# Optimization experiments

Hardware: AMD Instinct MI355X
Metric: run time of the kernel (lower is better)

The kernel has to match this reference:

```python
import jax, jax.numpy as jnp
import numpy as np

N, C, H, W = 8, 192, 112, 112
TEMPERATURE = 0.1


def setup_inputs() -> dict:
    key = jax.random.key(0)
    k1, k2 = jax.random.split(key)
    features = jax.random.normal(k1, (N, C, H, W), dtype=jnp.float32)
    # Raw per-pixel directions in {-1, 0, 1}; clip the neighbor coordinate into
    # bounds and recompute the direction so EVERY neighbor is valid. The torch
    # module's broadcasting (labels[:, i, j] vs an (N, M) gather) only works when
    # all N neighbors are valid at each pixel, so this matches its assumptions.
    raw = jax.random.randint(k2, (N, 2, H, W), -1, 2)
    ii = jnp.arange(H)[None, :, None]
    jj = jnp.arange(W)[None, None, :]
    d0 = jnp.clip(ii + raw[:, 0], 0, H - 1) - ii
    d1 = jnp.clip(jj + raw[:, 1], 0, W - 1) - jj
    directions = jnp.stack([d0, d1], axis=1).astype(jnp.int32)
    # Single-class labels: the original loss is -inf whenever any mask entry is 0
    # (log of exactly 0), so a finite, comparable baseline needs matching labels.
    labels = jnp.zeros((N, H, W), dtype=jnp.int32)
    return {"features": features, "labels": labels, "directions": directions}


def reference(features, labels, directions):
    # F.normalize(features, dim=1): x / max(||x||_2, eps)
    norm = jnp.linalg.norm(features, axis=1, keepdims=True)
    fn = features / jnp.maximum(norm, 1e-12)

    ii = jnp.arange(H)[None, :, None]
    jj = jnp.arange(W)[None, None, :]
    ni = ii + directions[:, 0]  # (N, H, W), in-bounds by construction
    nj = jj + directions[:, 1]  # (N, H, W)

    # Torch: features[:, :, neighbor_i, neighbor_j] gathers the M(==N) neighbor
    # coordinates across ALL batch elements -> (N, C, N, H, W) = [n, c, m, i, j]
    gathered = fn[:, :, ni, nj]
    # logits[n, m, i, j] = <fn[n, :, i, j], fn[n, :, ni[m,i,j], nj[m,i,j]]> / T
    logits = jnp.einsum('ncij,ncmij->nmij', fn, gathered) / TEMPERATURE

    # mask[n, m, i, j] = (labels[m, i, j] == labels[n, ni[m,i,j], nj[m,i,j]])
    # (torch broadcasts labels[:, i, j] along the first axis of the (N, M) gather)
    labels_g = labels[:, ni, nj]  # (N, N, H, W) = [n, m, i, j]
    mask = (labels[None, :, :, :] == labels_g).astype(fn.dtype)

    exp_l = jnp.exp(logits) * mask
    denom = jnp.sum(exp_l, axis=1, keepdims=True)  # sum over m
    # sum_{i,j} mean_{n,m}(.) / (H*W) == global mean over (n, m, i, j)
    loss = (-jnp.log(exp_l / (denom + 1e-6))).mean()
    return loss
```

## Files before the change

### kernel.cpp

```cpp
#include <hip/hip_runtime.h>
#include <math.h>


namespace {
constexpr int N_ = 8, C_ = 192, H_ = 112, W_ = 112;
constexpr int HW = H_ * W_;
constexpr int TH = 2;
constexpr int WSX = 56;
constexpr int TROWS = TH + 2;
constexpr int RS = WSX + 2;
constexpr int TILE_E = TROWS * RS;
constexpr int NT = 64;
constexpr int NS4 = TILE_E - 3 * NT;
constexpr int NPAIR = TH * (WSX / 2);
constexpr int KCH = 8;
constexpr int GRP = KCH / 2;
constexpr int NCHUNK = C_ / KCH;
constexpr int GX = W_ / WSX, GY = H_ / TH;
constexpr int NBLK = GX * GY * N_;
constexpr float INV_T = 10.0f;
constexpr double TOTAL = (double)N_ * N_ * H_ * W_;
}

__device__ __forceinline__ float sel3(int d, float a, float b, float c) {
    float r = (d < 0) ? a : b;
    return (d > 0) ? c : r;
}

__device__ __forceinline__ float px_loss(
    const float l[3][3], int gi, int gj, int n,
    const int* __restrict__ labels, const int* __restrict__ dirs)
{
    const int pix = gi * W_ + gj;
    float denom = 0.f, sumlog = 0.f;
#pragma unroll
    for (int m = 0; m < N_; ++m) {
        int d0 = dirs[((m * 2 + 0) * H_ + gi) * W_ + gj];
        int d1 = dirs[((m * 2 + 1) * H_ + gi) * W_ + gj];
        float r0 = sel3(d1, l[0][0], l[0][1], l[0][2]);
        float r1 = sel3(d1, l[1][0], l[1][1], l[1][2]);
        float r2 = sel3(d1, l[2][0], l[2][1], l[2][2]);
        float lm = sel3(d0, r0, r1, r2);
        int labm = labels[m * HW + pix];
        int labn = labels[n * HW + (gi + d0) * W_ + (gj + d1)];
        bool msk = (labm == labn);
        float e = msk ? __expf(lm) : 0.f;
        denom += e;
        sumlog += msk ? lm : -INFINITY;
    }
    return 8.0f * __logf(denom + 1e-6f) - sumlog;
}

extern "C" __global__ void __launch_bounds__(NT, 4)
dcl_main(const float* __restrict__ feat,
         const int* __restrict__ labels,
         const int* __restrict__ dirs,
         double* __restrict__ partial, int use_partial)
{
    alignas(16) __shared__ float2 tl[2 * GRP * TILE_E];
    __shared__ float ssb[TILE_E];

    const int lane = threadIdx.x;
    const int gx0 = blockIdx.x * WSX;
    const int gy0 = blockIdx.y * TH;
    const int n   = blockIdx.z;

    const bool has4 = (lane < NS4);
    int gofs[4];
    #pragma unroll
    for (int sI = 0; sI < 4; ++sI) {
        int s = lane + sI * NT;
        if (s >= TILE_E) s = TILE_E - 1;
        int r = s / RS, c = s - r * RS;
        gofs[sI] = min(max(gy0 + r - 1, 0), H_ - 1) * W_
                 + min(max(gx0 + c - 1, 0), W_ - 1);
    }

    const bool is_px = (lane < NPAIR);
    const int py  = lane / (WSX / 2);
    const int pxp = lane - py * (WSX / 2);
    const int wb  = py * RS + 2 * pxp;

    const float* __restrict__ plane = feat + (size_t)n * C_ * HW;

#define TLP(buf, g) (tl + ((buf) * GRP + (g)) * TILE_E)

    float sA[9], sB[9];
    #pragma unroll
    for (int k = 0; k < 9; ++k) { sA[k] = 0.f; sB[k] = 0.f; }
    float ss[4] = {0.f, 0.f, 0.f, 0.f};

    {
        float v[4][KCH];
        #pragma unroll
        for (int k = 0; k < KCH; ++k) {
            v[0][k] = plane[(size_t)k * HW + gofs[0]];
            v[1][k] = plane[(size_t)k * HW + gofs[1]];
            v[2][k] = plane[(size_t)k * HW + gofs[2]];
        }
        if (has4)
            #pragma unroll
            for (int k = 0; k < KCH; ++k) v[3][k] = plane[(size_t)k * HW + gofs[3]];
        #pragma unroll
        for (int g = 0; g < GRP; ++g) {
            TLP(0, g)[lane]            = make_float2(v[0][2*g], v[0][2*g+1]);
            TLP(0, g)[lane + NT]       = make_float2(v[1][2*g], v[1][2*g+1]);
            TLP(0, g)[lane + 2 * NT]   = make_float2(v[2][2*g], v[2][2*g+1]);
        }
        if (has4)
            #pragma unroll
            for (int g = 0; g < GRP; ++g)
                TLP(0, g)[lane + 3 * NT] = make_float2(v[3][2*g], v[3][2*g+1]);
        #pragma unroll
        for (int k = 0; k < KCH; ++k) {
            ss[0] = fmaf(v[0][k], v[0][k], ss[0]);
            ss[1] = fmaf(v[1][k], v[1][k], ss[1]);
            ss[2] = fmaf(v[2][k], v[2][k], ss[2]);
            if (has4) ss[3] = fmaf(v[3][k], v[3][k], ss[3]);
        }
    }
    __syncthreads();

    for (int t = 0; t < NCHUNK; ++t) {
        float v[4][KCH];
        const bool more = (t + 1 < NCHUNK);
        if (more) {
            const float* p = plane + (size_t)(t + 1) * KCH * HW;
            #pragma unroll
            for (int k = 0; k < KCH; ++k) {
                v[0][k] = p[(size_t)k * HW + gofs[0]];
                v[1][k] = p[(size_t)k * HW + gofs[1]];
                v[2][k] = p[(size_t)k * HW + gofs[2]];
            }
            if (has4)
                #pragma unroll
                for (int k = 0; k < KCH; ++k) v[3][k] = p[(size_t)k * HW + gofs[3]];
        }

        const int buf = t & 1;
        if (is_px) {
            #pragma unroll
            for (int g = 0; g < GRP; ++g) {
                const float2* __restrict__ cp = TLP(buf, g);
                float4 L0 = *reinterpret_cast<const float4*>(cp + wb);
                float4 R0 = *reinterpret_cast<const float4*>(cp + wb + 2);
                float4 L1 = *reinterpret_cast<const float4*>(cp + wb + RS);
                float4 R1 = *reinterpret_cast<const float4*>(cp + wb + RS + 2);
                float4 L2 = *reinterpret_cast<const float4*>(cp + wb + 2 * RS);
                float4 R2 = *reinterpret_cast<const float4*>(cp + wb + 2 * RS + 2);
                const float fAx = L1.z, fAy = L1.w;
                const float fBx = R1.x, fBy = R1.y;
                sA[0] = fmaf(fAx, L0.x, fmaf(fAy, L0.y, sA[0]));
                sA[1] = fmaf(fAx, L0.z, fmaf(fAy, L0.w, sA[1]));
                sA[2] = fmaf(fAx, R0.x, fmaf(fAy, R0.y, sA[2]));
                sA[3] = fmaf(fAx, L1.x, fmaf(fAy, L1.y, sA[3]));
                sA[4] = fmaf(fAx, L1.z, fmaf(fAy, L1.w, sA[4]));
                sA[5] = fmaf(fAx, R1.x, fmaf(fAy, R1.y, sA[5]));
                sA[6] = fmaf(fAx, L2.x, fmaf(fAy, L2.y, sA[6]));
                sA[7] = fmaf(fAx, L2.z, fmaf(fAy, L2.w, sA[7]));
                sA[8] = fmaf(fAx, R2.x, fmaf(fAy, R2.y, sA[8]));
                sB[0] = fmaf(fBx, L0.z, fmaf(fBy, L0.w, sB[0]));
                sB[1] = fmaf(fBx, R0.x, fmaf(fBy, R0.y, sB[1]));
                sB[2] = fmaf(fBx, R0.z, fmaf(fBy, R0.w, sB[2]));
                sB[3] = fmaf(fBx, L1.z, fmaf(fBy, L1.w, sB[3]));
                sB[4] = fmaf(fBx, R1.x, fmaf(fBy, R1.y, sB[4]));
                sB[5] = fmaf(fBx, R1.z, fmaf(fBy, R1.w, sB[5]));
                sB[6] = fmaf(fBx, L2.z, fmaf(fBy, L2.w, sB[6]));
                sB[7] = fmaf(fBx, R2.x, fmaf(fBy, R2.y, sB[7]));
                sB[8] = fmaf(fBx, R2.z, fmaf(fBy, R2.w, sB[8]));
            }
        }

        if (more) {
            const int nb = buf ^ 1;
            #pragma unroll
            for (int g = 0; g < GRP; ++g) {
                TLP(nb, g)[lane]          = make_float2(v[0][2*g], v[0][2*g+1]);
                TLP(nb, g)[lane + NT]     = make_float2(v[1][2*g], v[1][2*g+1]);
                TLP(nb, g)[lane + 2 * NT] = make_float2(v[2][2*g], v[2][2*g+1]);
            }
            if (has4)
                #pragma unroll
                for (int g = 0; g < GRP; ++g)
                    TLP(nb, g)[lane + 3 * NT] = make_float2(v[3][2*g], v[3][2*g+1]);
            #pragma unroll
            for (int k = 0; k < KCH; ++k) {
                ss[0] = fmaf(v[0][k], v[0][k], ss[0]);
                ss[1] = fmaf(v[1][k], v[1][k], ss[1]);
                ss[2] = fmaf(v[2][k], v[2][k], ss[2]);
                if (has4) ss[3] = fmaf(v[3][k], v[3][k], ss[3]);
            }
        }
        __syncthreads();
    }

    ssb[lane]          = 1.0f / fmaxf(sqrtf(ss[0]), 1e-12f);
    ssb[lane + NT]     = 1.0f / fmaxf(sqrtf(ss[1]), 1e-12f);
    ssb[lane + 2 * NT] = 1.0f / fmaxf(sqrtf(ss[2]), 1e-12f);
    if (has4) ssb[lane + 3 * NT] = 1.0f / fmaxf(sqrtf(ss[3]), 1e-12f);
    __syncthreads();

    float lp = 0.0f;
    if (is_px) {
        float iv[3][4];
        #pragma unroll
        for (int r = 0; r < 3; ++r)
            #pragma unroll
            for (int c = 0; c < 4; ++c)
                iv[r][c] = ssb[wb + r * RS + c];
        const float iA = iv[1][1] * INV_T, iB = iv[1][2] * INV_T;
        float lA[3][3], lB[3][3];
        #pragma unroll
        for (int r = 0; r < 3; ++r)
            #pragma unroll
            for (int c = 0; c < 3; ++c) {
                lA[r][c] = sA[r * 3 + c] * iA * iv[r][c];
                lB[r][c] = sB[r * 3 + c] * iB * iv[r][c + 1];
            }
        const int gi = gy0 + py, gj = gx0 + 2 * pxp;
        lp = px_loss(lA, gi, gj, n, labels, dirs)
           + px_loss(lB, gi, gj + 1, n, labels, dirs);
    }
    #pragma unroll
    for (int off = 32; off > 0; off >>= 1) lp += __shfl_down(lp, off, 64);
    if (lane == 0) {
        const int bid = (blockIdx.z * gridDim.y + blockIdx.y) * gridDim.x + blockIdx.x;
        if (use_partial) partial[bid] = (double)lp;
        else atomicAdd(partial, (double)lp);
    }
#undef TLP
}

extern "C" __global__ void __launch_bounds__(256)
dcl_final(const double* __restrict__ partial, float* __restrict__ out, int nblk)
{
    const int tid = threadIdx.x;
    double s = 0.0;
    for (int i = tid; i < nblk; i += 256) s += partial[i];
    #pragma unroll
    for (int off = 32; off > 0; off >>= 1) s += __shfl_down(s, off, 64);
    __shared__ double red[4];
    const int lane = tid & 63, wv = tid >> 6;
    if (lane == 0) red[wv] = s;
    __syncthreads();
    if (tid == 0) out[0] = (float)((red[0] + red[1] + red[2] + red[3]) / TOTAL);
}

extern "C" void kernel_launch(void* const* d_in, const int* in_sizes, int n_in,
                              void* d_out, int out_size, void* d_ws, size_t ws_size,
                              hipStream_t stream) {
    const float* feat   = (const float*)d_in[0];
    const int*   labels = (const int*)d_in[1];
    const int*   dirs   = (const int*)d_in[2];
    double* acc = (double*)d_ws;
    float*  out = (float*)d_out;

    const int use_partial = (ws_size >= (size_t)NBLK * sizeof(double)) ? 1 : 0;
    if (!use_partial) hipMemsetAsync(acc, 0, sizeof(double), stream);
    dim3 grid(GX, GY, N_);
    dcl_main<<<grid, NT, 0, stream>>>(feat, labels, dirs, acc, use_partial);
    dcl_final<<<1, 256, 0, stream>>>(acc, out, use_partial ? NBLK : 1);
}
```

Baseline: 130.9 us.

## Split channel reduction across four wavefronts per block with shared-memory combine

Each block now runs 256 threads, and each of its four wavefronts handles a quarter of the channels using private double-buffered tiles. Because the buffers are per-wave, the per-chunk __syncthreads is dropped. Partial dot products and squared norms are written to shared memory and summed across waves before the loss epilogue, which is also split across waves. This aims to raise memory-level parallelism and shorten the serial channel loop, at the cost of extra shared memory, cross-wave reduction and a second block-level sync.

```diff
diff --git a/kernel.cpp b/kernel.cpp
--- a/kernel.cpp
+++ b/kernel.cpp
@@ -7,15 +7,16 @@
 constexpr int HW = H_ * W_;
 constexpr int TH = 2;
 constexpr int WSX = 56;
-constexpr int TROWS = TH + 2;
-constexpr int RS = WSX + 2;
-constexpr int TILE_E = TROWS * RS;
-constexpr int NT = 64;
-constexpr int NS4 = TILE_E - 3 * NT;
-constexpr int NPAIR = TH * (WSX / 2);
-constexpr int KCH = 8;
-constexpr int GRP = KCH / 2;
-constexpr int NCHUNK = C_ / KCH;
+constexpr int RS = 58;
+constexpr int TILE_E = 4 * RS;
+constexpr int NT = 256;
+constexpr int NWV = 4;
+constexpr int CW = C_ / NWV;
+constexpr int KCH = 2;
+constexpr int NCHUNK = CW / KCH;
+constexpr int NS4 = TILE_E - 3 * 64;
+constexpr int NPAIR = 56;
+constexpr int EXS = 19;
 constexpr int GX = W_ / WSX, GY = H_ / TH;
 constexpr int NBLK = GX * GY * N_;
 constexpr float INV_T = 10.0f;
@@ -57,10 +58,15 @@
          const int* __restrict__ dirs,
          double* __restrict__ partial, int use_partial)
 {
-    alignas(16) __shared__ float2 tl[2 * GRP * TILE_E];
+    alignas(16) __shared__ float2 tl[NWV * 2 * TILE_E];
+    __shared__ float ex[NWV * NPAIR * EXS];
+    __shared__ float ssq[NWV * TILE_E];
     __shared__ float ssb[TILE_E];
-
-    const int lane = threadIdx.x;
+    __shared__ float red[NWV];
+
+    const int tid  = threadIdx.x;
+    const int lane = tid & 63;
+    const int wv   = tid >> 6;
     const int gx0 = blockIdx.x * WSX;
     const int gy0 = blockIdx.y * TH;
     const int n   = blockIdx.z;
@@ -69,7 +75,7 @@
     int gofs[4];
     #pragma unroll
     for (int sI = 0; sI < 4; ++sI) {
-        int s = lane + sI * NT;
+        int s = lane + sI * 64;
         if (s >= TILE_E) s = TILE_E - 1;
         int r = s / RS, c = s - r * RS;
         gofs[sI] = min(max(gy0 + r - 1, 0), H_ - 1) * W_
@@ -81,9 +87,9 @@
     const int pxp = lane - py * (WSX / 2);
     const int wb  = py * RS + 2 * pxp;
 
-    const float* __restrict__ plane = feat + (size_t)n * C_ * HW;
-
-#define TLP(buf, g) (tl + ((buf) * GRP + (g)) * TILE_E)
+    const float* __restrict__ wplane =
+        feat + ((size_t)n * C_ + (size_t)wv * CW) * HW;
+    float2* __restrict__ mytl = tl + wv * 2 * TILE_E;
 
     float sA[9], sB[9];
     #pragma unroll
@@ -91,144 +97,138 @@
     float ss[4] = {0.f, 0.f, 0.f, 0.f};
 
     {
-        float v[4][KCH];
-        #pragma unroll
-        for (int k = 0; k < KCH; ++k) {
-            v[0][k] = plane[(size_t)k * HW + gofs[0]];
-            v[1][k] = plane[(size_t)k * HW + gofs[1]];
-            v[2][k] = plane[(size_t)k * HW + gofs[2]];
-        }
-        if (has4)
-            #pragma unroll
-            for (int k = 0; k < KCH; ++k) v[3][k] = plane[(size_t)k * HW + gofs[3]];
-        #pragma unroll
-        for (int g = 0; g < GRP; ++g) {
-            TLP(0, g)[lane]            = make_float2(v[0][2*g], v[0][2*g+1]);
-            TLP(0, g)[lane + NT]       = make_float2(v[1][2*g], v[1][2*g+1]);
-            TLP(0, g)[lane + 2 * NT]   = make_float2(v[2][2*g], v[2][2*g+1]);
-        }
-        if (has4)
-            #pragma unroll
-            for (int g = 0; g < GRP; ++g)
-                TLP(0, g)[lane + 3 * NT] = make_float2(v[3][2*g], v[3][2*g+1]);
-        #pragma unroll
-        for (int k = 0; k < KCH; ++k) {
-            ss[0] = fmaf(v[0][k], v[0][k], ss[0]);
-            ss[1] = fmaf(v[1][k], v[1][k], ss[1]);
-            ss[2] = fmaf(v[2][k], v[2][k], ss[2]);
-            if (has4) ss[3] = fmaf(v[3][k], v[3][k], ss[3]);
-        }
-    }
-    __syncthreads();
+        float a[4], b[4];
+        #pragma unroll
+        for (int i = 0; i < 3; ++i) { a[i] = wplane[gofs[i]]; b[i] = wplane[HW + gofs[i]]; }
+        if (has4) { a[3] = wplane[gofs[3]]; b[3] = wplane[HW + gofs[3]]; }
+        #pragma unroll
+        for (int i = 0; i < 3; ++i) {
+            mytl[lane + i * 64] = make_float2(a[i], b[i]);
+            ss[i] = fmaf(a[i], a[i], fmaf(b[i], b[i], ss[i]));
+        }
+        if (has4) {
+            mytl[lane + 192] = make_float2(a[3], b[3]);
+            ss[3] = fmaf(a[3], a[3], fmaf(b[3], b[3], ss[3]));
+        }
+    }
 
     for (int t = 0; t < NCHUNK; ++t) {
-        float v[4][KCH];
+        float a[4], b[4];
         const bool more = (t + 1 < NCHUNK);
         if (more) {
-            const float* p = plane + (size_t)(t + 1) * KCH * HW;
-            #pragma unroll
-            for (int k = 0; k < KCH; ++k) {
-                v[0][k] = p[(size_t)k * HW + gofs[0]];
-                v[1][k] = p[(size_t)k * HW + gofs[1]];
-                v[2][k] = p[(size_t)k * HW + gofs[2]];
+            const float* __restrict__ p = wplane + (size_t)(t + 1) * KCH * HW;
+            #pragma unroll
+            for (int i = 0; i < 3; ++i) { a[i] = p[gofs[i]]; b[i] = p[HW + gofs[i]]; }
+            if (has4) { a[3] = p[gofs[3]]; b[3] = p[HW + gofs[3]]; }
+        }
+
+        if (is_px) {
+            const float2* __restrict__ cp = mytl + (t & 1) * TILE_E;
+            float4 L0 = *reinterpret_cast<const float4*>(cp + wb);
+            float4 R0 = *reinterpret_cast<const float4*>(cp + wb + 2);
+            float4 L1 = *reinterpret_cast<const float4*>(cp + wb + RS);
+            float4 R1 = *reinterpret_cast<const float4*>(cp + wb + RS + 2);
+            float4 L2 = *reinterpret_cast<const float4*>(cp + wb + 2 * RS);
+            float4 R2 = *reinterpret_cast<const float4*>(cp + wb + 2 * RS + 2);
+            const float fAx = L1.z, fAy = L1.w;
+            const float fBx = R1.x, fBy = R1.y;
+            sA[0] = fmaf(fAx, L0.x, fmaf(fAy, L0.y, sA[0]));
+            sA[1] = fmaf(fAx, L0.z, fmaf(fAy, L0.w, sA[1]));
+            sA[2] = fmaf(fAx, R0.x, fmaf(fAy, R0.y, sA[2]));
+            sA[3] = fmaf(fAx, L1.x, fmaf(fAy, L1.y, sA[3]));
+            sA[4] = fmaf(fAx, L1.z, fmaf(fAy, L1.w, sA[4]));
+            sA[5] = fmaf(fAx, R1.x, fmaf(fAy, R1.y, sA[5]));
+            sA[6] = fmaf(fAx, L2.x, fmaf(fAy, L2.y, sA[6]));
+            sA[7] = fmaf(fAx, L2.z, fmaf(fAy, L2.w, sA[7]));
+            sA[8] = fmaf(fAx, R2.x, fmaf(fAy, R2.y, sA[8]));
+            sB[0] = fmaf(fBx, L0.z, fmaf(fBy, L0.w, sB[0]));
+            sB[1] = fmaf(fBx, R0.x, fmaf(fBy, R0.y, sB[1]));
+            sB[2] = fmaf(fBx, R0.z, fmaf(fBy, R0.w, sB[2]));
+            sB[3] = fmaf(fBx, L1.z, fmaf(fBy, L1.w, sB[3]));
+            sB[4] = fmaf(fBx, R1.x, fmaf(fBy, R1.y, sB[4]));
+            sB[5] = fmaf(fBx, R1.z, fmaf(fBy, R1.w, sB[5]));
+            sB[6] = fmaf(fBx, L2.z, fmaf(fBy, L2.w, sB[6]));
+            sB[7] = fmaf(fBx, R2.x, fmaf(fBy, R2.y, sB[7]));
+            sB[8] = fmaf(fBx, R2.z, fmaf(fBy, R2.w, sB[8]));
+        }
+
+        if (more) {
+            float2* __restrict__ np = mytl + ((t + 1) & 1) * TILE_E;
+            #pragma unroll
+            for (int i = 0; i < 3; ++i) {
+                np[lane + i * 64] = make_float2(a[i], b[i]);
+                ss[i] = fmaf(a[i], a[i], fmaf(b[i], b[i], ss[i]));
             }
-            if (has4)
-                #pragma unroll
-                for (int k = 0; k < KCH; ++k) v[3][k] = p[(size_t)k * HW + gofs[3]];
-        }
-
-        const int buf = t & 1;
-        if (is_px) {
-            #pragma unroll
-            for (int g = 0; g < GRP; ++g) {
-                const float2* __restrict__ cp = TLP(buf, g);
-                float4 L0 = *reinterpret_cast<const float4*>(cp + wb);
-                float4 R0 = *reinterpret_cast<const float4*>(cp + wb + 2);
-                float4 L1 = *reinterpret_cast<const float4*>(cp + wb + RS);
-                float4 R1 = *reinterpret_cast<const float4*>(cp + wb + RS + 2);
-                float4 L2 = *reinterpret_cast<const float4*>(cp + wb + 2 * RS);
-                float4 R2 = *reinterpret_cast<const float4*>(cp + wb + 2 * RS + 2);
-                const float fAx = L1.z, fAy = L1.w;
-                const float fBx = R1.x, fBy = R1.y;
-                sA[0] = fmaf(fAx, L0.x, fmaf(fAy, L0.y, sA[0]));
-                sA[1] = fmaf(fAx, L0.z, fmaf(fAy, L0.w, sA[1]));
-                sA[2] = fmaf(fAx, R0.x, fmaf(fAy, R0.y, sA[2]));
-                sA[3] = fmaf(fAx, L1.x, fmaf(fAy, L1.y, sA[3]));
-                sA[4] = fmaf(fAx, L1.z, fmaf(fAy, L1.w, sA[4]));
-                sA[5] = fmaf(fAx, R1.x, fmaf(fAy, R1.y, sA[5]));
-                sA[6] = fmaf(fAx, L2.x, fmaf(fAy, L2.y, sA[6]));
-                sA[7] = fmaf(fAx, L2.z, fmaf(fAy, L2.w, sA[7]));
-                sA[8] = fmaf(fAx, R2.x, fmaf(fAy, R2.y, sA[8]));
-                sB[0] = fmaf(fBx, L0.z, fmaf(fBy, L0.w, sB[0]));
-                sB[1] = fmaf(fBx, R0.x, fmaf(fBy, R0.y, sB[1]));
-                sB[2] = fmaf(fBx, R0.z, fmaf(fBy, R0.w, sB[2]));
-                sB[3] = fmaf(fBx, L1.z, fmaf(fBy, L1.w, sB[3]));
-                sB[4] = fmaf(fBx, R1.x, fmaf(fBy, R1.y, sB[4]));
-                sB[5] = fmaf(fBx, R1.z, fmaf(fBy, R1.w, sB[5]));
-                sB[6] = fmaf(fBx, L2.z, fmaf(fBy, L2.w, sB[6]));
-                sB[7] = fmaf(fBx, R2.x, fmaf(fBy, R2.y, sB[7]));
-                sB[8] = fmaf(fBx, R2.z, fmaf(fBy, R2.w, sB[8]));
+            if (has4) {
+                np[lane + 192] = make_float2(a[3], b[3]);
+                ss[3] = fmaf(a[3], a[3], fmaf(b[3], b[3], ss[3]));
             }
         }
-
-        if (more) {
-            const int nb = buf ^ 1;
-            #pragma unroll
-            for (int g = 0; g < GRP; ++g) {
-                TLP(nb, g)[lane]          = make_float2(v[0][2*g], v[0][2*g+1]);
-                TLP(nb, g)[lane + NT]     = make_float2(v[1][2*g], v[1][2*g+1]);
-                TLP(nb, g)[lane + 2 * NT] = make_float2(v[2][2*g], v[2][2*g+1]);
-            }
-            if (has4)
-                #pragma unroll
-                for (int g = 0; g < GRP; ++g)
-                    TLP(nb, g)[lane + 3 * NT] = make_float2(v[3][2*g], v[3][2*g+1]);
-            #pragma unroll
-            for (int k = 0; k < KCH; ++k) {
-                ss[0] = fmaf(v[0][k], v[0][k], ss[0]);
-                ss[1] = fmaf(v[1][k], v[1][k], ss[1]);
-                ss[2] = fmaf(v[2][k], v[2][k], ss[2]);
-                if (has4) ss[3] = fmaf(v[3][k], v[3][k], ss[3]);
-            }
-        }
-        __syncthreads();
-    }
-
-    ssb[lane]          = 1.0f / fmaxf(sqrtf(ss[0]), 1e-12f);
-    ssb[lane + NT]     = 1.0f / fmaxf(sqrtf(ss[1]), 1e-12f);
-    ssb[lane + 2 * NT] = 1.0f / fmaxf(sqrtf(ss[2]), 1e-12f);
-    if (has4) ssb[lane + 3 * NT] = 1.0f / fmaxf(sqrtf(ss[3]), 1e-12f);
+    }
+
+    ssq[wv * TILE_E + lane]       = ss[0];
+    ssq[wv * TILE_E + lane + 64]  = ss[1];
+    ssq[wv * TILE_E + lane + 128] = ss[2];
+    if (has4) ssq[wv * TILE_E + lane + 192] = ss[3];
+    if (is_px) {
+        float* e = ex + (wv * NPAIR + lane) * EXS;
+        #pragma unroll
+        for (int k = 0; k < 9; ++k) { e[k] = sA[k]; e[9 + k] = sB[k]; }
+    }
+    __syncthreads();
+
+    if (tid < TILE_E) {
+        float t = ssq[tid] + ssq[TILE_E + tid]
+                + ssq[2 * TILE_E + tid] + ssq[3 * TILE_E + tid];
+        ssb[tid] = 1.0f / fmaxf(sqrtf(t), 1e-12f);
+    }
     __syncthreads();
 
     float lp = 0.0f;
-    if (is_px) {
+    if (lane < NPAIR / NWV) {
+        const int pr  = wv * (NPAIR / NWV) + lane;
+        const int ppy = pr / (WSX / 2);
+        const int ppx = pr - ppy * (WSX / 2);
+        const int wbs = ppy * RS + 2 * ppx;
+
+        float sa[9], sb[9];
+        #pragma unroll
+        for (int k = 0; k < 9; ++k) { sa[k] = 0.f; sb[k] = 0.f; }
+        #pragma unroll
+        for (int w = 0; w < NWV; ++w) {
+            const float* e = ex + (w * NPAIR + pr) * EXS;
+            #pragma unroll
+            for (int k = 0; k < 9; ++k) { sa[k] += e[k]; sb[k] += e[9 + k]; }
+        }
         float iv[3][4];
         #pragma unroll
         for (int r = 0; r < 3; ++r)
             #pragma unroll
             for (int c = 0; c < 4; ++c)
-                iv[r][c] = ssb[wb + r * RS + c];
+                iv[r][c] = ssb[wbs + r * RS + c];
         const float iA = iv[1][1] * INV_T, iB = iv[1][2] * INV_T;
         float lA[3][3], lB[3][3];
         #pragma unroll
         for (int r = 0; r < 3; ++r)
             #pragma unroll
             for (int c = 0; c < 3; ++c) {
-                lA[r][c] = sA[r * 3 + c] * iA * iv[r][c];
-                lB[r][c] = sB[r * 3 + c] * iB * iv[r][c + 1];
+                lA[r][c] = sa[r * 3 + c] * iA * iv[r][c];
+                lB[r][c] = sb[r * 3 + c] * iB * iv[r][c + 1];
             }
-        const int gi = gy0 + py, gj = gx0 + 2 * pxp;
+        const int gi = gy0 + ppy, gj = gx0 + 2 * ppx;
         lp = px_loss(lA, gi, gj, n, labels, dirs)
            + px_loss(lB, gi, gj + 1, n, labels, dirs);
     }
     #pragma unroll
     for (int off = 32; off > 0; off >>= 1) lp += __shfl_down(lp, off, 64);
-    if (lane == 0) {
+    if (lane == 0) red[wv] = lp;
+    __syncthreads();
+    if (tid == 0) {
         const int bid = (blockIdx.z * gridDim.y + blockIdx.y) * gridDim.x + blockIdx.x;
-        if (use_partial) partial[bid] = (double)lp;
-        else atomicAdd(partial, (double)lp);
-    }
-#undef TLP
+        float t = red[0] + red[1] + red[2] + red[3];
+        if (use_partial) partial[bid] = (double)t;
+        else atomicAdd(partial, (double)t);
+    }
 }
 
 extern "C" __global__ void __launch_bounds__(256)
```

Result: slower. 134.0 us (+2.4%).
